# Kernel optimization log

Hardware: AMD Instinct MI355X
Metric: run time of the kernel (lower is better)

Reference implementation:

```python
import jax, jax.numpy as jnp
import numpy as np

N = 50000
E = 800000
IN_F = 128
HID_F = 128
OUT_F = 64


def setup_inputs() -> dict:
    key = jax.random.key(0)
    ks = jax.random.split(key, 12)
    x = jax.random.normal(ks[0], (N, IN_F), dtype=jnp.float32)
    row0 = jax.random.randint(ks[1], (E,), 0, N, dtype=jnp.int32)
    col0 = jax.random.randint(ks[2], (E,), 0, N, dtype=jnp.int32)
    val0 = jax.random.uniform(ks[3], (E,), dtype=jnp.float32)
    row1 = jax.random.randint(ks[4], (E,), 0, N, dtype=jnp.int32)
    col1 = jax.random.randint(ks[5], (E,), 0, N, dtype=jnp.int32)
    val1 = jax.random.uniform(ks[6], (E,), dtype=jnp.float32)
    # GraphConvolution params, uniform(-stdv, stdv) with stdv = 1/sqrt(out_features)
    s0 = 1.0 / np.sqrt(HID_F)
    W0 = jax.random.uniform(ks[7], (IN_F, HID_F), minval=-s0, maxval=s0, dtype=jnp.float32)
    b0 = jax.random.uniform(ks[8], (HID_F,), minval=-s0, maxval=s0, dtype=jnp.float32)
    s1 = 1.0 / np.sqrt(OUT_F)
    W1 = jax.random.uniform(ks[9], (HID_F, OUT_F), minval=-s1, maxval=s1, dtype=jnp.float32)
    b1 = jax.random.uniform(ks[10], (OUT_F,), minval=-s1, maxval=s1, dtype=jnp.float32)
    return {"x": x, "row0": row0, "col0": col0, "val0": val0,
            "row1": row1, "col1": col1, "val1": val1,
            "W0": W0, "b0": b0, "W1": W1, "b1": b1}


def _gcn_layer(x, W, b, row, col, val):
    # support = x @ W ; out = spmm(adj, support) + b
    support = x @ W                       # [N, F_out]
    msgs = val[:, None] * support[col]    # [E, F_out] gather along edges
    out = jax.ops.segment_sum(msgs, row, num_segments=N)
    return out + b


def reference(x, row0, col0, val0, row1, col1, val1, W0, b0, W1, b1):
    # Layer 0: GC -> relu (dropout is identity in eval mode)
    h = _gcn_layer(x, W0, b0, row0, col0, val0)
    h = jax.nn.relu(h)
    # Layer 1 (final): GC only
    out = _gcn_layer(h, W1, b1, row1, col1, val1)
    return out
```

## Files before the change

kernel.cpp:

```cpp
#include <hip/hip_runtime.h>
#include <hip/hip_fp16.h>

#define N_NODES 50000
#define IN_F    128
#define HID_F   128
#define OUT_F   64
#define E_EDGES 800000

#define RPB   128
#define NBUCK ((N_NODES + RPB - 1) / RPB)
#define BCAP  2560
#define BIN_T   512
#define BIN_EPT 8
#define BIN_EPB (BIN_T * BIN_EPT)
#define BIN_NB  ((E_EDGES + BIN_EPB - 1) / BIN_EPB)

typedef _Float16 half8 __attribute__((ext_vector_type(8)));
typedef float    floatx4 __attribute__((ext_vector_type(4)));

__global__ void convert_x_kernel(const float* __restrict__ x, __half* __restrict__ y, int n4) {
    int i = blockIdx.x * 256 + threadIdx.x;
    if (i < n4) {
        float4 v = ((const float4*)x)[i];
        ((__half2*)y)[2 * i + 0] = __floats2half2_rn(v.x, v.y);
        ((__half2*)y)[2 * i + 1] = __floats2half2_rn(v.z, v.w);
    }
}

__global__ void convert_w_kernel(const float* __restrict__ W0, const float* __restrict__ W1,
                                 __half* __restrict__ wt0, __half* __restrict__ wt1) {
    int tid = blockIdx.x * 256 + threadIdx.x;
    if (blockIdx.y == 0) {
        if (tid < IN_F * HID_F) {
            int k = tid >> 7, n = tid & 127;
            wt0[n * IN_F + k] = __float2half(W0[tid]);
        }
    } else {
        if (tid < HID_F * OUT_F) {
            int k = tid / OUT_F, n = tid % OUT_F;
            wt1[n * HID_F + k] = __float2half(W1[tid]);
        }
    }
}

template<int K, int NF, bool RELU_A>
__global__ __launch_bounds__(256) void gemm_mfma_kernel(const __half* __restrict__ A,
                                                        const __half* __restrict__ Wt,
                                                        __half* __restrict__ C, int M) {
    constexpr int KP = K + 8;
    constexpr int NT = NF / 16;
    __shared__ _Float16 Ws[NF * KP];
    const int tid = threadIdx.x;
    constexpr int CH = NF * K / 8;
    for (int c = tid; c < CH; c += 256) {
        const int n = c / (K / 8), ko = (c % (K / 8)) * 8;
        *(half8*)&Ws[n * KP + ko] = *(const half8*)(Wt + n * K + ko);
    }
    __syncthreads();

    const int wv = tid >> 6, lane = tid & 63;
    const int quad = lane >> 4, l16 = lane & 15;
    const int rowb = blockIdx.x * 64 + wv * 16;
    const int arow = rowb + l16;

    floatx4 acc[NT] = {};
#pragma unroll
    for (int ks = 0; ks < K; ks += 32) {
        half8 af = {};
        if (arow < M) af = *(const half8*)(A + (long)arow * K + ks + quad * 8);
        if (RELU_A) {
            _Float16 z = (_Float16)0;
#pragma unroll
            for (int j = 0; j < 8; ++j) af[j] = af[j] > z ? af[j] : z;
        }
#pragma unroll
        for (int t = 0; t < NT; ++t) {
            half8 bf = *(const half8*)&Ws[(t * 16 + l16) * KP + ks + quad * 8];
            acc[t] = __builtin_amdgcn_mfma_f32_16x16x32_f16(af, bf, acc[t], 0, 0, 0);
        }
    }
#pragma unroll
    for (int t = 0; t < NT; ++t) {
        const int col = t * 16 + l16;
#pragma unroll
        for (int i = 0; i < 4; ++i) {
            const int row = rowb + quad * 4 + i;
            if (row < M) C[(long)row * NF + col] = __float2half(acc[t][i]);
        }
    }
}

__global__ void zero_int_kernel(int* __restrict__ p, int n) {
    int tid = blockIdx.x * blockDim.x + threadIdx.x;
    if (tid < n) p[tid] = 0;
}

__global__ __launch_bounds__(BIN_T) void bin_kernel(
        const int* __restrict__ row0, const int* __restrict__ col0, const float* __restrict__ val0,
        const int* __restrict__ row1, const int* __restrict__ col1, const float* __restrict__ val1,
        int* __restrict__ gfill, int2* __restrict__ bcv0, int2* __restrict__ bcv1) {
    const int g = blockIdx.y;
    const int*   rowi = g ? row1 : row0;
    const int*   coli = g ? col1 : col0;
    const float* vali = g ? val1 : val0;
    int*  gf  = gfill + g * NBUCK;
    int2* bcv = g ? bcv1 : bcv0;

    __shared__ int lhist[NBUCK];
    __shared__ int lbase[NBUCK];
    const int tid = threadIdx.x;
    for (int i = tid; i < NBUCK; i += BIN_T) lhist[i] = 0;
    __syncthreads();

    int rnk[BIN_EPT], bkt[BIN_EPT], cl[BIN_EPT], rw[BIN_EPT];
    float vl[BIN_EPT];
    const int e0 = blockIdx.x * BIN_EPB;
#pragma unroll
    for (int i = 0; i < BIN_EPT; ++i) {
        const int e = e0 + i * BIN_T + tid;
        bkt[i] = -1;
        if (e < E_EDGES) {
            const int r = rowi[e];
            rw[i] = r; cl[i] = coli[e]; vl[i] = vali[e];
            const int b = r / RPB;
            bkt[i] = b;
            rnk[i] = atomicAdd(&lhist[b], 1);
        }
    }
    __syncthreads();
    for (int i = tid; i < NBUCK; i += BIN_T) {
        const int c = lhist[i];
        lbase[i] = c ? atomicAdd(&gf[i], c) : 0;
    }
    __syncthreads();
#pragma unroll
    for (int i = 0; i < BIN_EPT; ++i) {
        if (bkt[i] >= 0) {
            const int pos = lbase[bkt[i]] + rnk[i];
            if (pos < BCAP)
                bcv[(long)bkt[i] * BCAP + pos] =
                    make_int2(((rw[i] & (RPB - 1)) << 16) | cl[i], __float_as_int(vl[i]));
        }
    }
}

__global__ __launch_bounds__(256) void sort_kernel(const int* __restrict__ gfill,
                                                   int2* __restrict__ bcv0,
                                                   int2* __restrict__ bcv1,
                                                   int* __restrict__ rs0,
                                                   int* __restrict__ rs1) {
    const int g = blockIdx.y;
    const int b = blockIdx.x;
    int2* buf = (g ? bcv1 : bcv0) + (long)b * BCAP;
    int*  rs  = (g ? rs1 : rs0) + b * (RPB + 1);

    __shared__ int2 sbuf[BCAP];
    __shared__ int  cur[RPB];
    __shared__ int  sc[RPB];
    __shared__ int  start[RPB + 1];

    const int tid = threadIdx.x;
    int cnt = gfill[g * NBUCK + b];
    if (cnt > BCAP) cnt = BCAP;

    if (tid < RPB) cur[tid] = 0;
    __syncthreads();
    for (int e = tid; e < cnt; e += 256)
        atomicAdd(&cur[buf[e].x >> 16], 1);
    __syncthreads();
    if (tid < RPB) sc[tid] = cur[tid];
    __syncthreads();
    for (int off = 1; off < RPB; off <<= 1) {
        int v = 0;
        if (tid < RPB && tid >= off) v = sc[tid - off];
        __syncthreads();
        if (tid < RPB) sc[tid] += v;
        __syncthreads();
    }
    if (tid < RPB) {
        start[tid + 1] = sc[tid];
        if (tid == 0) start[0] = 0;
        cur[tid] = (tid == 0) ? 0 : sc[tid - 1];
    }
    __syncthreads();
    for (int e = tid; e < cnt; e += 256) {
        int2 r = buf[e];
        int pos = atomicAdd(&cur[r.x >> 16], 1);
        sbuf[pos] = r;
    }
    __syncthreads();
    for (int e = tid; e < cnt; e += 256) buf[e] = sbuf[e];
    for (int i = tid; i <= RPB; i += 256) rs[i] = start[i];
}

template<int F, int VEC, bool OUT_HALF>
__global__ __launch_bounds__(256) void spmm_kernel(const int* __restrict__ rs,
                                                   const int2* __restrict__ bcv,
                                                   const __half* __restrict__ sup,
                                                   const float* __restrict__ bias,
                                                   void* __restrict__ outv, int n) {
    static_assert(F == 64 * VEC, "one wave per row");
    const int wave = threadIdx.x >> 6;
    const int lane = threadIdx.x & 63;
    const int r = blockIdx.x * 4 + wave;
    if (r >= n) return;
    const int b  = r >> 7;
    const int rl = r & (RPB - 1);
    const int* rsb = rs + b * (RPB + 1);
    const int start = rsb[rl];
    const int end   = rsb[rl + 1];
    const int2* eb = bcv + (long)b * BCAP;
    const int f0 = lane * VEC;
    float acc0 = bias[f0];
    float acc1 = (VEC == 2) ? bias[f0 + 1] : 0.f;

    for (int base = start; base < end; base += 64) {
        const int m = min(64, end - base);
        int2 cvl = make_int2(0, 0);
        if (lane < m) cvl = eb[base + lane];
        int j = 0;
        for (; j + 4 <= m; j += 4) {
            const int   p0 = __shfl(cvl.x, j + 0, 64);
            const float v0 = __int_as_float(__shfl(cvl.y, j + 0, 64));
            const int   p1 = __shfl(cvl.x, j + 1, 64);
            const float v1 = __int_as_float(__shfl(cvl.y, j + 1, 64));
            const int   p2 = __shfl(cvl.x, j + 2, 64);
            const float v2 = __int_as_float(__shfl(cvl.y, j + 2, 64));
            const int   p3 = __shfl(cvl.x, j + 3, 64);
            const float v3 = __int_as_float(__shfl(cvl.y, j + 3, 64));
            if constexpr (VEC == 2) {
                __half2 s0 = *(const __half2*)(sup + (long)(p0 & 0xFFFF) * F + f0);
                __half2 s1 = *(const __half2*)(sup + (long)(p1 & 0xFFFF) * F + f0);
                __half2 s2 = *(const __half2*)(sup + (long)(p2 & 0xFFFF) * F + f0);
                __half2 s3 = *(const __half2*)(sup + (long)(p3 & 0xFFFF) * F + f0);
                float2 g0 = __half22float2(s0), g1 = __half22float2(s1);
                float2 g2 = __half22float2(s2), g3 = __half22float2(s3);
                acc0 += v0 * g0.x; acc1 += v0 * g0.y;
                acc0 += v1 * g1.x; acc1 += v1 * g1.y;
                acc0 += v2 * g2.x; acc1 += v2 * g2.y;
                acc0 += v3 * g3.x; acc1 += v3 * g3.y;
            } else {
                float s0 = __half2float(sup[(long)(p0 & 0xFFFF) * F + f0]);
                float s1 = __half2float(sup[(long)(p1 & 0xFFFF) * F + f0]);
                float s2 = __half2float(sup[(long)(p2 & 0xFFFF) * F + f0]);
                float s3 = __half2float(sup[(long)(p3 & 0xFFFF) * F + f0]);
                acc0 += v0 * s0 + v1 * s1 + v2 * s2 + v3 * s3;
            }
        }
        for (; j < m; ++j) {
            const int   p = __shfl(cvl.x, j, 64);
            const float v = __int_as_float(__shfl(cvl.y, j, 64));
            if constexpr (VEC == 2) {
                float2 g = __half22float2(*(const __half2*)(sup + (long)(p & 0xFFFF) * F + f0));
                acc0 += v * g.x; acc1 += v * g.y;
            } else {
                acc0 += v * __half2float(sup[(long)(p & 0xFFFF) * F + f0]);
            }
        }
    }
    if constexpr (OUT_HALF) {
        __half* out = (__half*)outv;
        *(__half2*)(out + (long)r * F + f0) = __floats2half2_rn(acc0, acc1);
    } else {
        float* out = (float*)outv;
        out[(long)r * F + f0] = acc0;
    }
}

extern "C" void kernel_launch(void* const* d_in, const int* in_sizes, int n_in,
                              void* d_out, int out_size, void* d_ws, size_t ws_size,
                              hipStream_t stream) {
    const float* x    = (const float*)d_in[0];
    const int*   row0 = (const int*)d_in[1];
    const int*   col0 = (const int*)d_in[2];
    const float* val0 = (const float*)d_in[3];
    const int*   row1 = (const int*)d_in[4];
    const int*   col1 = (const int*)d_in[5];
    const float* val1 = (const float*)d_in[6];
    const float* W0   = (const float*)d_in[7];
    const float* b0   = (const float*)d_in[8];
    const float* W1   = (const float*)d_in[9];
    const float* b1   = (const float*)d_in[10];
    float* out = (float*)d_out;

    const int M = N_NODES;

    __half* x16  = (__half*)d_ws;
    __half* sup0 = x16 + (long)N_NODES * IN_F;
    __half* h    = sup0 + (long)N_NODES * HID_F;
    int2* bcv0   = (int2*)(h + (long)N_NODES * HID_F);
    int2* bcv1   = bcv0 + (long)NBUCK * BCAP;
    int*  rs0    = (int*)(bcv1 + (long)NBUCK * BCAP);
    int*  rs1    = rs0 + NBUCK * (RPB + 1);
    int*  gfill  = rs1 + NBUCK * (RPB + 1);
    __half* wt0  = (__half*)(gfill + 2 * NBUCK + 2);
    __half* wt1  = wt0 + IN_F * HID_F;
    __half* sup1 = sup0;

    const int SPMM_B = (N_NODES + 3) / 4;

    zero_int_kernel<<<(2 * NBUCK + 255) / 256, 256, 0, stream>>>(gfill, 2 * NBUCK);
    convert_x_kernel<<<(N_NODES * IN_F / 4 + 255) / 256, 256, 0, stream>>>(x, x16, N_NODES * IN_F / 4);
    convert_w_kernel<<<dim3(64, 2), 256, 0, stream>>>(W0, W1, wt0, wt1);
    bin_kernel<<<dim3(BIN_NB, 2), BIN_T, 0, stream>>>(row0, col0, val0, row1, col1, val1,
                                                      gfill, bcv0, bcv1);
    sort_kernel<<<dim3(NBUCK, 2), 256, 0, stream>>>(gfill, bcv0, bcv1, rs0, rs1);

    gemm_mfma_kernel<IN_F, HID_F, false><<<(M + 63) / 64, 256, 0, stream>>>(x16, wt0, sup0, M);
    spmm_kernel<HID_F, 2, true><<<SPMM_B, 256, 0, stream>>>(rs0, bcv0, sup0, b0, h, N_NODES);

    gemm_mfma_kernel<HID_F, OUT_F, true><<<(M + 63) / 64, 256, 0, stream>>>(h, wt1, sup1, M);
    spmm_kernel<OUT_F, 1, false><<<SPMM_B, 256, 0, stream>>>(rs1, bcv1, sup1, b1, out, N_NODES);
}
```

Before: 204.2 us.

## Fuse x conversion into GEMM, merge prep kernels, widen sort and SpMM unroll

The first GEMM now reads fp32 x directly and converts to fp16 in registers, which removes the separate convert_x pass and its fp16 intermediate buffer. The weight conversion and the bucket-counter zeroing are merged into one prep kernel, cutting two launches. The sort kernel uses 512 threads, and the SpMM inner loop now issues 8 independent gathers per iteration instead of 4 to raise memory-level parallelism. The GEMM loads twice the bytes of A per fragment, and the wider unroll adds register pressure.

```diff
diff --git a/kernel.cpp b/kernel.cpp
--- a/kernel.cpp
+++ b/kernel.cpp
@@ -1,5 +1,6 @@
 #include <hip/hip_runtime.h>
 #include <hip/hip_fp16.h>
+#include <type_traits>
 
 #define N_NODES 50000
 #define IN_F    128
@@ -18,33 +19,25 @@
 typedef _Float16 half8 __attribute__((ext_vector_type(8)));
 typedef float    floatx4 __attribute__((ext_vector_type(4)));
 
-__global__ void convert_x_kernel(const float* __restrict__ x, __half* __restrict__ y, int n4) {
-    int i = blockIdx.x * 256 + threadIdx.x;
-    if (i < n4) {
-        float4 v = ((const float4*)x)[i];
-        ((__half2*)y)[2 * i + 0] = __floats2half2_rn(v.x, v.y);
-        ((__half2*)y)[2 * i + 1] = __floats2half2_rn(v.z, v.w);
-    }
-}
-
-__global__ void convert_w_kernel(const float* __restrict__ W0, const float* __restrict__ W1,
-                                 __half* __restrict__ wt0, __half* __restrict__ wt1) {
+__global__ __launch_bounds__(256) void prep_kernel(const float* __restrict__ W0,
+                                                   const float* __restrict__ W1,
+                                                   __half* __restrict__ wt0,
+                                                   __half* __restrict__ wt1,
+                                                   int* __restrict__ gfill) {
     int tid = blockIdx.x * 256 + threadIdx.x;
-    if (blockIdx.y == 0) {
-        if (tid < IN_F * HID_F) {
-            int k = tid >> 7, n = tid & 127;
-            wt0[n * IN_F + k] = __float2half(W0[tid]);
-        }
-    } else {
-        if (tid < HID_F * OUT_F) {
-            int k = tid / OUT_F, n = tid % OUT_F;
-            wt1[n * HID_F + k] = __float2half(W1[tid]);
-        }
-    }
-}
-
-template<int K, int NF, bool RELU_A>
-__global__ __launch_bounds__(256) void gemm_mfma_kernel(const __half* __restrict__ A,
+    if (tid < IN_F * HID_F) {
+        int k = tid >> 7, n = tid & 127;
+        wt0[n * IN_F + k] = __float2half(W0[tid]);
+    }
+    if (tid < HID_F * OUT_F) {
+        int k = tid / OUT_F, n = tid % OUT_F;
+        wt1[n * HID_F + k] = __float2half(W1[tid]);
+    }
+    if (tid < 2 * NBUCK) gfill[tid] = 0;
+}
+
+template<int K, int NF, bool RELU_A, typename AT>
+__global__ __launch_bounds__(256) void gemm_mfma_kernel(const AT* __restrict__ A,
                                                         const __half* __restrict__ Wt,
                                                         __half* __restrict__ C, int M) {
     constexpr int KP = K + 8;
@@ -67,7 +60,18 @@
 #pragma unroll
     for (int ks = 0; ks < K; ks += 32) {
         half8 af = {};
-        if (arow < M) af = *(const half8*)(A + (long)arow * K + ks + quad * 8);
+        if (arow < M) {
+            if constexpr (std::is_same<AT, float>::value) {
+                const float4* p = (const float4*)(A + (long)arow * K + ks + quad * 8);
+                float4 u = p[0], w = p[1];
+                af[0] = (_Float16)u.x; af[1] = (_Float16)u.y;
+                af[2] = (_Float16)u.z; af[3] = (_Float16)u.w;
+                af[4] = (_Float16)w.x; af[5] = (_Float16)w.y;
+                af[6] = (_Float16)w.z; af[7] = (_Float16)w.w;
+            } else {
+                af = *(const half8*)(A + (long)arow * K + ks + quad * 8);
+            }
+        }
         if (RELU_A) {
             _Float16 z = (_Float16)0;
 #pragma unroll
@@ -88,11 +92,6 @@
             if (row < M) C[(long)row * NF + col] = __float2half(acc[t][i]);
         }
     }
-}
-
-__global__ void zero_int_kernel(int* __restrict__ p, int n) {
-    int tid = blockIdx.x * blockDim.x + threadIdx.x;
-    if (tid < n) p[tid] = 0;
 }
 
 __global__ __launch_bounds__(BIN_T) void bin_kernel(
@@ -144,11 +143,12 @@
     }
 }
 
-__global__ __launch_bounds__(256) void sort_kernel(const int* __restrict__ gfill,
-                                                   int2* __restrict__ bcv0,
-                                                   int2* __restrict__ bcv1,
-                                                   int* __restrict__ rs0,
-                                                   int* __restrict__ rs1) {
+#define SORT_T 512
+__global__ __launch_bounds__(SORT_T) void sort_kernel(const int* __restrict__ gfill,
+                                                      int2* __restrict__ bcv0,
+                                                      int2* __restrict__ bcv1,
+                                                      int* __restrict__ rs0,
+                                                      int* __restrict__ rs1) {
     const int g = blockIdx.y;
     const int b = blockIdx.x;
     int2* buf = (g ? bcv1 : bcv0) + (long)b * BCAP;
@@ -165,7 +165,7 @@
 
     if (tid < RPB) cur[tid] = 0;
     __syncthreads();
-    for (int e = tid; e < cnt; e += 256)
+    for (int e = tid; e < cnt; e += SORT_T)
         atomicAdd(&cur[buf[e].x >> 16], 1);
     __syncthreads();
     if (tid < RPB) sc[tid] = cur[tid];
@@ -183,14 +183,14 @@
         cur[tid] = (tid == 0) ? 0 : sc[tid - 1];
     }
     __syncthreads();
-    for (int e = tid; e < cnt; e += 256) {
+    for (int e = tid; e < cnt; e += SORT_T) {
         int2 r = buf[e];
         int pos = atomicAdd(&cur[r.x >> 16], 1);
         sbuf[pos] = r;
     }
     __syncthreads();
-    for (int e = tid; e < cnt; e += 256) buf[e] = sbuf[e];
-    for (int i = tid; i <= RPB; i += 256) rs[i] = start[i];
+    for (int e = tid; e < cnt; e += SORT_T) buf[e] = sbuf[e];
+    for (int i = tid; i <= RPB; i += SORT_T) rs[i] = start[i];
 }
 
 template<int F, int VEC, bool OUT_HALF>
@@ -219,32 +219,31 @@
         int2 cvl = make_int2(0, 0);
         if (lane < m) cvl = eb[base + lane];
         int j = 0;
-        for (; j + 4 <= m; j += 4) {
-            const int   p0 = __shfl(cvl.x, j + 0, 64);
-            const float v0 = __int_as_float(__shfl(cvl.y, j + 0, 64));
-            const int   p1 = __shfl(cvl.x, j + 1, 64);
-            const float v1 = __int_as_float(__shfl(cvl.y, j + 1, 64));
-            const int   p2 = __shfl(cvl.x, j + 2, 64);
-            const float v2 = __int_as_float(__shfl(cvl.y, j + 2, 64));
-            const int   p3 = __shfl(cvl.x, j + 3, 64);
-            const float v3 = __int_as_float(__shfl(cvl.y, j + 3, 64));
+        for (; j + 8 <= m; j += 8) {
+            int   p[8];
+            float v[8];
+#pragma unroll
+            for (int q = 0; q < 8; ++q) {
+                p[q] = __shfl(cvl.x, j + q, 64);
+                v[q] = __int_as_float(__shfl(cvl.y, j + q, 64));
+            }
             if constexpr (VEC == 2) {
-                __half2 s0 = *(const __half2*)(sup + (long)(p0 & 0xFFFF) * F + f0);
-                __half2 s1 = *(const __half2*)(sup + (long)(p1 & 0xFFFF) * F + f0);
-                __half2 s2 = *(const __half2*)(sup + (long)(p2 & 0xFFFF) * F + f0);
-                __half2 s3 = *(const __half2*)(sup + (long)(p3 & 0xFFFF) * F + f0);
-                float2 g0 = __half22float2(s0), g1 = __half22float2(s1);
-                float2 g2 = __half22float2(s2), g3 = __half22float2(s3);
-                acc0 += v0 * g0.x; acc1 += v0 * g0.y;
-                acc0 += v1 * g1.x; acc1 += v1 * g1.y;
-                acc0 += v2 * g2.x; acc1 += v2 * g2.y;
-                acc0 += v3 * g3.x; acc1 += v3 * g3.y;
+                __half2 s[8];
+#pragma unroll
+                for (int q = 0; q < 8; ++q)
+                    s[q] = *(const __half2*)(sup + (long)(p[q] & 0xFFFF) * F + f0);
+#pragma unroll
+                for (int q = 0; q < 8; ++q) {
+                    float2 gq = __half22float2(s[q]);
+                    acc0 += v[q] * gq.x; acc1 += v[q] * gq.y;
+                }
             } else {
-                float s0 = __half2float(sup[(long)(p0 & 0xFFFF) * F + f0]);
-                float s1 = __half2float(sup[(long)(p1 & 0xFFFF) * F + f0]);
-                float s2 = __half2float(sup[(long)(p2 & 0xFFFF) * F + f0]);
-                float s3 = __half2float(sup[(long)(p3 & 0xFFFF) * F + f0]);
-                acc0 += v0 * s0 + v1 * s1 + v2 * s2 + v3 * s3;
+                float s[8];
+#pragma unroll
+                for (int q = 0; q < 8; ++q)
+                    s[q] = __half2float(sup[(long)(p[q] & 0xFFFF) * F + f0]);
+#pragma unroll
+                for (int q = 0; q < 8; ++q) acc0 += v[q] * s[q];
             }
         }
         for (; j < m; ++j) {
@@ -285,8 +284,7 @@
 
     const int M = N_NODES;
 
-    __half* x16  = (__half*)d_ws;
-    __half* sup0 = x16 + (long)N_NODES * IN_F;
+    __half* sup0 = (__half*)d_ws;
     __half* h    = sup0 + (long)N_NODES * HID_F;
     int2* bcv0   = (int2*)(h + (long)N_NODES * HID_F);
     int2* bcv1   = bcv0 + (long)NBUCK * BCAP;
@@ -299,16 +297,14 @@
 
     const int SPMM_B = (N_NODES + 3) / 4;
 
-    zero_int_kernel<<<(2 * NBUCK + 255) / 256, 256, 0, stream>>>(gfill, 2 * NBUCK);
-    convert_x_kernel<<<(N_NODES * IN_F / 4 + 255) / 256, 256, 0, stream>>>(x, x16, N_NODES * IN_F / 4);
-    convert_w_kernel<<<dim3(64, 2), 256, 0, stream>>>(W0, W1, wt0, wt1);
+    prep_kernel<<<(IN_F * HID_F + 255) / 256, 256, 0, stream>>>(W0, W1, wt0, wt1, gfill);
     bin_kernel<<<dim3(BIN_NB, 2), BIN_T, 0, stream>>>(row0, col0, val0, row1, col1, val1,
                                                       gfill, bcv0, bcv1);
-    sort_kernel<<<dim3(NBUCK, 2), 256, 0, stream>>>(gfill, bcv0, bcv1, rs0, rs1);
-
-    gemm_mfma_kernel<IN_F, HID_F, false><<<(M + 63) / 64, 256, 0, stream>>>(x16, wt0, sup0, M);
+    sort_kernel<<<dim3(NBUCK, 2), SORT_T, 0, stream>>>(gfill, bcv0, bcv1, rs0, rs1);
+
+    gemm_mfma_kernel<IN_F, HID_F, false, float><<<(M + 63) / 64, 256, 0, stream>>>(x, wt0, sup0, M);
     spmm_kernel<HID_F, 2, true><<<SPMM_B, 256, 0, stream>>>(rs0, bcv0, sup0, b0, h, N_NODES);
 
-    gemm_mfma_kernel<HID_F, OUT_F, true><<<(M + 63) / 64, 256, 0, stream>>>(h, wt1, sup1, M);
+    gemm_mfma_kernel<HID_F, OUT_F, true, __half><<<(M + 63) / 64, 256, 0, stream>>>(h, wt1, sup1, M);
     spmm_kernel<OUT_F, 1, false><<<SPMM_B, 256, 0, stream>>>(rs1, bcv1, sup1, b1, out, N_NODES);
 }
```

After: 198.3 us. 2.9% less time.
